# Optimization experiments

Measured on AMD Instinct MI355X. Metric: run time of the kernel, lower is better.

## Reference

```python
import jax, jax.numpy as jnp
import numpy as np

B, S, I, H = 1024, 1024, 32, 128

def setup_inputs() -> dict:
    key = jax.random.key(0)
    ks = jax.random.split(key, 10)
    def xavier(k, shape):
        fan_in, fan_out = shape
        bound = float(np.sqrt(6.0 / (fan_in + fan_out)))
        return jax.random.uniform(k, shape, jnp.float32, -bound, bound)
    return {
        "x": jax.random.normal(ks[0], (B, S, I), jnp.float32),
        "W_r": xavier(ks[1], (I, H)), "U_r": xavier(ks[2], (H, H)), "b_r": jnp.zeros((H,), jnp.float32),
        "W_z": xavier(ks[3], (I, H)), "U_z": xavier(ks[4], (H, H)), "b_z": jnp.zeros((H,), jnp.float32),
        "W_h": xavier(ks[5], (I, H)), "U_h": xavier(ks[6], (H, H)), "b_h": jnp.zeros((H,), jnp.float32),
    }

def reference(x, W_r, U_r, b_r, W_z, U_z, b_z, W_h, U_h, b_h):
    # x: [B, S, I]. Precompute all input projections in one big GEMM each (math-identical,
    # since x_t @ W is independent across t), then scan the sequential recurrence.
    xz = jnp.einsum('bsi,ih->bsh', x, W_z) + b_z  # [B,S,H]
    xh = jnp.einsum('bsi,ih->bsh', x, W_h) + b_h  # [B,S,H]
    # r_t = sigmoid(x@W_r + h@U_r + b_r) is computed in the original but never used
    # (h_tilde is NOT gated by r), so it has no effect on the output.

    h0 = jnp.zeros((x.shape[0], U_z.shape[0]), x.dtype)  # [B,H]

    def step(h, inp):
        xz_t, xh_t = inp  # each [B,H]
        z = jax.nn.sigmoid(xz_t + h @ U_z)
        hh = jnp.tanh(xh_t + h @ U_h)
        h_new = (1.0 - z) * h + z * hh  # note: swapped vs standard GRU, faithful to source
        return h_new, h_new

    # scan over time: [S,B,H]
    xs = (jnp.swapaxes(xz, 0, 1), jnp.swapaxes(xh, 0, 1))
    h_last, hs = jax.lax.scan(step, h0, xs)
    hidden_seq = jnp.swapaxes(hs, 0, 1)  # [B,S,H]
    return hidden_seq, h_last[None]  # final state keeps leading dim of 1, as in source
```

## Files before the change

### kernel.cpp

```cpp
#include <hip/hip_runtime.h>
#include <hip/hip_bf16.h>

typedef __bf16 bf16x8 __attribute__((ext_vector_type(8)));
typedef float  f32x4  __attribute__((ext_vector_type(4)));
typedef unsigned short u16;
typedef unsigned short u16x4 __attribute__((ext_vector_type(4)));
typedef unsigned long long u64;

#define NB 1024
#define NS 1024
#define NI 32
#define NH 128

__device__ __forceinline__ u64 pack4_bf16(f32x4 v) {
  u16x4 p;
#pragma unroll
  for (int r = 0; r < 4; ++r) p[r] = __builtin_bit_cast(u16, (__bf16)v[r]);
  return __builtin_bit_cast(u64, p);
}

__device__ __forceinline__ void lds_barrier() {
  __builtin_amdgcn_sched_barrier(0);
  asm volatile("s_waitcnt lgkmcnt(0)" ::: "memory");
  __builtin_amdgcn_s_barrier();
  asm volatile("" ::: "memory");
  __builtin_amdgcn_sched_barrier(0);
}

__global__ __launch_bounds__(512, 2) void gru_scan(
    const float* __restrict__ x,
    const float* __restrict__ Wz, const float* __restrict__ Uz, const float* __restrict__ bz,
    const float* __restrict__ Wh, const float* __restrict__ Uh, const float* __restrict__ bh,
    float* __restrict__ out)
{
  __shared__ __align__(16) u64 hb[2][16][17][2];
  __shared__ __align__(16) u64 hx[2][8][4][17][2];

  const int tid  = threadIdx.x;
  const int lane = tid & 63;
  const int w    = tid >> 6;
  const int ml   = lane & 15;
  const int g    = lane >> 4;
  const int rb   = blockIdx.x * 16;

  bf16x8 ufrag[2][4];
  bf16x8 wfrag[2];
  f32x4  bias2[2];
  {
    const float* Ug[2] = {Uz, Uh};
    const float* Wg[2] = {Wz, Wh};
    const float* bg[2] = {bz, bh};
    const int n0 = 16 * w + ml;
#pragma unroll
    for (int gate = 0; gate < 2; ++gate) {
#pragma unroll
      for (int kt = 0; kt < 4; ++kt)
#pragma unroll
        for (int j = 0; j < 8; ++j)
          ufrag[gate][kt][j] = (__bf16)Ug[gate][(32 * kt + 8 * g + j) * NH + n0];
#pragma unroll
      for (int j = 0; j < 8; ++j)
        wfrag[gate][j] = (__bf16)Wg[gate][(8 * g + j) * NH + n0];
      const int nb = 16 * w + 4 * g;
#pragma unroll
      for (int r = 0; r < 4; ++r) bias2[gate][r] = bg[gate][nb + r];
    }
  }

  for (int i = tid; i < 16 * 17 * 2; i += 512) ((u64*)hb[0])[i] = 0ULL;

  const int r_st  = tid >> 5;
  const int c8    = tid & 31;
  const int tt_st = c8 >> 2;
  const int ku_st = c8 & 3;
  const float* xbase = x + (size_t)(rb + r_st) * (NS * NI) + c8 * 8;

  {
    f32x4 a0 = *(const f32x4*)(xbase);
    f32x4 a1 = *(const f32x4*)(xbase + 4);
    bf16x8 u;
#pragma unroll
    for (int j = 0; j < 4; ++j) { u[j] = (__bf16)a0[j]; u[4 + j] = (__bf16)a1[j]; }
    *(bf16x8*)&hx[0][tt_st][ku_st][r_st][0] = u;
  }
  __syncthreads();

  const int woff_ku = 2 * w + (g >> 1);
  const int whalf   = g & 1;

  f32x4 hv = {0.f, 0.f, 0.f, 0.f};
  float* optr = out + (size_t)(rb + ml) * NS * NH + 16 * w + 4 * g;

  f32x4 vxa, vxb;
  const float NL2E  = -1.4426950408889634f;
  const float P2L2E =  2.8853900817779268f;
  const f32x4 zero4 = {0.f, 0.f, 0.f, 0.f};

  f32x4 axz, axh;
  {
    bf16x8 xf = *(const bf16x8*)&hx[0][0][g][ml][0];
    axz = __builtin_amdgcn_mfma_f32_16x16x32_bf16(wfrag[0], xf, bias2[0], 0, 0, 0);
    axh = __builtin_amdgcn_mfma_f32_16x16x32_bf16(wfrag[1], xf, bias2[1], 0, 0, 0);
  }

#define GRU_STEP(P, XB, TT)                                                                \
  {                                                                                        \
                      \
    bf16x8 hf0 = *(const bf16x8*)&hb[P][ 0 + g][ml][0];                                    \
    bf16x8 hf1 = *(const bf16x8*)&hb[P][ 4 + g][ml][0];                                    \
    bf16x8 hf2 = *(const bf16x8*)&hb[P][ 8 + g][ml][0];                                    \
    bf16x8 hf3 = *(const bf16x8*)&hb[P][12 + g][ml][0];                                    \
    const int nxb = ((TT) == 7) ? (XB) ^ 1 : (XB);                                         \
    const int ntt = ((TT) + 1) & 7;                                                        \
    bf16x8 xf = *(const bf16x8*)&hx[nxb][ntt][g][ml][0];                                   \
                                         \
    f32x4 z1 = __builtin_amdgcn_mfma_f32_16x16x32_bf16(ufrag[0][0], hf0, axz,   0, 0, 0);  \
    f32x4 h1 = __builtin_amdgcn_mfma_f32_16x16x32_bf16(ufrag[1][0], hf0, axh,   0, 0, 0);  \
    f32x4 z2 = __builtin_amdgcn_mfma_f32_16x16x32_bf16(ufrag[0][2], hf2, zero4, 0, 0, 0);  \
    f32x4 h2 = __builtin_amdgcn_mfma_f32_16x16x32_bf16(ufrag[1][2], hf2, zero4, 0, 0, 0);  \
    z1 = __builtin_amdgcn_mfma_f32_16x16x32_bf16(ufrag[0][1], hf1, z1, 0, 0, 0);           \
    h1 = __builtin_amdgcn_mfma_f32_16x16x32_bf16(ufrag[1][1], hf1, h1, 0, 0, 0);           \
    z2 = __builtin_amdgcn_mfma_f32_16x16x32_bf16(ufrag[0][3], hf3, z2, 0, 0, 0);           \
    h2 = __builtin_amdgcn_mfma_f32_16x16x32_bf16(ufrag[1][3], hf3, h2, 0, 0, 0);           \
                                    \
    axz = __builtin_amdgcn_mfma_f32_16x16x32_bf16(wfrag[0], xf, bias2[0], 0, 0, 0);        \
    axh = __builtin_amdgcn_mfma_f32_16x16x32_bf16(wfrag[1], xf, bias2[1], 0, 0, 0);        \
    const f32x4 az = z1 + z2;                                                              \
    const f32x4 ah = h1 + h2;                                                              \
                                        \
    f32x4 hn;                                                                              \
    _Pragma("unroll")                                                                      \
    for (int r = 0; r < 4; ++r) {                                                          \
      float ez = __builtin_amdgcn_exp2f(az[r] * NL2E);                                     \
      float zz = __builtin_amdgcn_rcpf(1.f + ez);                                          \
      float eh = __builtin_amdgcn_exp2f(ah[r] * P2L2E);                                    \
      float th = 1.f - 2.f * __builtin_amdgcn_rcpf(1.f + eh);                              \
      hn[r] = __builtin_fmaf(zz, th - hv[r], hv[r]);                                       \
    }                                                                                      \
    hv = hn;                                                                               \
                                              \
    hb[P ^ 1][woff_ku][ml][whalf] = pack4_bf16(hn);                                        \
                      \
    __builtin_nontemporal_store(hn, (f32x4*)optr);                                         \
    optr += NH;                                                                            \
  }

  for (int chunk = 0; chunk < NS / 8; ++chunk) {
    const int  xb   = chunk & 1;
    const bool more = (chunk + 1 < NS / 8);
#pragma unroll
    for (int tt = 0; tt < 8; ++tt) {
      if (tt == 0 && more) {
        const float* p = xbase + (size_t)(chunk + 1) * (8 * NI);
        vxa = *(const f32x4*)(p);
        vxb = *(const f32x4*)(p + 4);
      }

      if (tt & 1) { GRU_STEP(1, xb, tt) } else { GRU_STEP(0, xb, tt) }

      if (tt == 6 && more) {
        bf16x8 u;
#pragma unroll
        for (int j = 0; j < 4; ++j) { u[j] = (__bf16)vxa[j]; u[4 + j] = (__bf16)vxb[j]; }
        *(bf16x8*)&hx[xb ^ 1][tt_st][ku_st][r_st][0] = u;
      }

      lds_barrier();
    }
  }

  const size_t lbase = (size_t)NB * NS * NH + (size_t)(rb + ml) * NH + 16 * w + 4 * g;
  *(f32x4*)(out + lbase) = hv;
}

extern "C" void kernel_launch(void* const* d_in, const int* in_sizes, int n_in,
                              void* d_out, int out_size, void* d_ws, size_t ws_size,
                              hipStream_t stream) {
  const float* x  = (const float*)d_in[0];
  const float* Wz = (const float*)d_in[4];
  const float* Uz = (const float*)d_in[5];
  const float* bz = (const float*)d_in[6];
  const float* Wh = (const float*)d_in[7];
  const float* Uh = (const float*)d_in[8];
  const float* bh = (const float*)d_in[9];
  float* out = (float*)d_out;

  gru_scan<<<dim3(NB / 16), dim3(512), 0, stream>>>(x, Wz, Uz, bz, Wh, Uh, bh, out);
}
```

Before: 490.6 us.

## Halve block to 4 waves with two column tiles each and fuse gate math

Each block now runs 256 threads (4 waves), and each wave computes two 16-column output tiles per gate instead of one. The aim is cheaper per-step barriers and more MFMA work per wave to hide latency on the sequential scan. The gate math is rewritten to use a single reciprocal by combining sigmoid and tanh into one fraction, with inputs clamped to ±15 to avoid overflow. In exchange, each wave holds more register fragments and there are fewer waves per CU to overlap stalls.

Measured after the change: 572.9 us. +16.8%, slower.

```diff
diff --git a/kernel.cpp b/kernel.cpp
--- a/kernel.cpp
+++ b/kernel.cpp
@@ -27,7 +27,26 @@
   __builtin_amdgcn_sched_barrier(0);
 }
 
-__global__ __launch_bounds__(512, 2) void gru_scan(
+__device__ __forceinline__ f32x4 gru_elem(f32x4 az, f32x4 ah, f32x4 h) {
+  const float NL2E  = -1.4426950408889634f;
+  const float P2L2E =  2.8853900817779268f;
+  f32x4 hn;
+#pragma unroll
+  for (int r = 0; r < 4; ++r) {
+    float a  = fminf(15.f, fmaxf(-15.f, az[r]));
+    float b  = fminf(15.f, fmaxf(-15.f, ah[r]));
+    float e  = __builtin_amdgcn_exp2f(a * NL2E);
+    float f  = __builtin_amdgcn_exp2f(b * P2L2E);
+    float fp = f + 1.f;
+    float num = __builtin_fmaf(-h[r], fp, f - 1.f);
+    float den = (1.f + e) * fp;
+    float rr  = __builtin_amdgcn_rcpf(den);
+    hn[r] = __builtin_fmaf(num, rr, h[r]);
+  }
+  return hn;
+}
+
+__global__ __launch_bounds__(256, 1) void gru_scan(
     const float* __restrict__ x,
     const float* __restrict__ Wz, const float* __restrict__ Uz, const float* __restrict__ bz,
     const float* __restrict__ Wh, const float* __restrict__ Uh, const float* __restrict__ bh,
@@ -43,106 +62,119 @@
   const int g    = lane >> 4;
   const int rb   = blockIdx.x * 16;
 
-  bf16x8 ufrag[2][4];
-  bf16x8 wfrag[2];
-  f32x4  bias2[2];
+  bf16x8 ufrag[2][2][4];
+  bf16x8 wfrag[2][2];
+  f32x4  bias2[2][2];
   {
     const float* Ug[2] = {Uz, Uh};
     const float* Wg[2] = {Wz, Wh};
     const float* bg[2] = {bz, bh};
-    const int n0 = 16 * w + ml;
 #pragma unroll
     for (int gate = 0; gate < 2; ++gate) {
 #pragma unroll
-      for (int kt = 0; kt < 4; ++kt)
+      for (int nt = 0; nt < 2; ++nt) {
+        const int n0 = 32 * w + 16 * nt + ml;
+#pragma unroll
+        for (int kt = 0; kt < 4; ++kt)
+#pragma unroll
+          for (int j = 0; j < 8; ++j)
+            ufrag[gate][nt][kt][j] = (__bf16)Ug[gate][(32 * kt + 8 * g + j) * NH + n0];
 #pragma unroll
         for (int j = 0; j < 8; ++j)
-          ufrag[gate][kt][j] = (__bf16)Ug[gate][(32 * kt + 8 * g + j) * NH + n0];
-#pragma unroll
-      for (int j = 0; j < 8; ++j)
-        wfrag[gate][j] = (__bf16)Wg[gate][(8 * g + j) * NH + n0];
-      const int nb = 16 * w + 4 * g;
-#pragma unroll
-      for (int r = 0; r < 4; ++r) bias2[gate][r] = bg[gate][nb + r];
+          wfrag[gate][nt][j] = (__bf16)Wg[gate][(8 * g + j) * NH + n0];
+        const int nb = 32 * w + 16 * nt + 4 * g;
+#pragma unroll
+        for (int r = 0; r < 4; ++r) bias2[gate][nt][r] = bg[gate][nb + r];
+      }
     }
   }
 
-  for (int i = tid; i < 16 * 17 * 2; i += 512) ((u64*)hb[0])[i] = 0ULL;
-
-  const int r_st  = tid >> 5;
-  const int c8    = tid & 31;
-  const int tt_st = c8 >> 2;
-  const int ku_st = c8 & 3;
-  const float* xbase = x + (size_t)(rb + r_st) * (NS * NI) + c8 * 8;
+  for (int i = tid; i < 16 * 17 * 2; i += 256) ((u64*)hb[0])[i] = 0ULL;
+
+  const int r_st  = tid >> 4;
+  const int c16   = tid & 15;
+  const int tt_st = c16 >> 1;
+  const int ku0   = (c16 & 1) * 2;
+  const float* xbase = x + (size_t)(rb + r_st) * (NS * NI) + tt_st * NI + (c16 & 1) * 16;
 
   {
     f32x4 a0 = *(const f32x4*)(xbase);
     f32x4 a1 = *(const f32x4*)(xbase + 4);
-    bf16x8 u;
-#pragma unroll
-    for (int j = 0; j < 4; ++j) { u[j] = (__bf16)a0[j]; u[4 + j] = (__bf16)a1[j]; }
-    *(bf16x8*)&hx[0][tt_st][ku_st][r_st][0] = u;
+    f32x4 a2 = *(const f32x4*)(xbase + 8);
+    f32x4 a3 = *(const f32x4*)(xbase + 12);
+    bf16x8 u0, u1;
+#pragma unroll
+    for (int j = 0; j < 4; ++j) {
+      u0[j] = (__bf16)a0[j]; u0[4 + j] = (__bf16)a1[j];
+      u1[j] = (__bf16)a2[j]; u1[4 + j] = (__bf16)a3[j];
+    }
+    *(bf16x8*)&hx[0][tt_st][ku0 + 0][r_st][0] = u0;
+    *(bf16x8*)&hx[0][tt_st][ku0 + 1][r_st][0] = u1;
   }
   __syncthreads();
 
-  const int woff_ku = 2 * w + (g >> 1);
-  const int whalf   = g & 1;
-
-  f32x4 hv = {0.f, 0.f, 0.f, 0.f};
-  float* optr = out + (size_t)(rb + ml) * NS * NH + 16 * w + 4 * g;
-
-  f32x4 vxa, vxb;
-  const float NL2E  = -1.4426950408889634f;
-  const float P2L2E =  2.8853900817779268f;
+  f32x4 hv0 = {0.f, 0.f, 0.f, 0.f};
+  f32x4 hv1 = {0.f, 0.f, 0.f, 0.f};
+  float* optr = out + (size_t)(rb + ml) * NS * NH + 32 * w + 4 * g;
+
+  f32x4 vx0, vx1, vx2, vx3;
   const f32x4 zero4 = {0.f, 0.f, 0.f, 0.f};
 
-  f32x4 axz, axh;
+  f32x4 axz0, axz1, axh0, axh1;
   {
     bf16x8 xf = *(const bf16x8*)&hx[0][0][g][ml][0];
-    axz = __builtin_amdgcn_mfma_f32_16x16x32_bf16(wfrag[0], xf, bias2[0], 0, 0, 0);
-    axh = __builtin_amdgcn_mfma_f32_16x16x32_bf16(wfrag[1], xf, bias2[1], 0, 0, 0);
-  }
-
-#define GRU_STEP(P, XB, TT)                                                                \
-  {                                                                                        \
-                      \
-    bf16x8 hf0 = *(const bf16x8*)&hb[P][ 0 + g][ml][0];                                    \
-    bf16x8 hf1 = *(const bf16x8*)&hb[P][ 4 + g][ml][0];                                    \
-    bf16x8 hf2 = *(const bf16x8*)&hb[P][ 8 + g][ml][0];                                    \
-    bf16x8 hf3 = *(const bf16x8*)&hb[P][12 + g][ml][0];                                    \
-    const int nxb = ((TT) == 7) ? (XB) ^ 1 : (XB);                                         \
-    const int ntt = ((TT) + 1) & 7;                                                        \
-    bf16x8 xf = *(const bf16x8*)&hx[nxb][ntt][g][ml][0];                                   \
-                                         \
-    f32x4 z1 = __builtin_amdgcn_mfma_f32_16x16x32_bf16(ufrag[0][0], hf0, axz,   0, 0, 0);  \
-    f32x4 h1 = __builtin_amdgcn_mfma_f32_16x16x32_bf16(ufrag[1][0], hf0, axh,   0, 0, 0);  \
-    f32x4 z2 = __builtin_amdgcn_mfma_f32_16x16x32_bf16(ufrag[0][2], hf2, zero4, 0, 0, 0);  \
-    f32x4 h2 = __builtin_amdgcn_mfma_f32_16x16x32_bf16(ufrag[1][2], hf2, zero4, 0, 0, 0);  \
-    z1 = __builtin_amdgcn_mfma_f32_16x16x32_bf16(ufrag[0][1], hf1, z1, 0, 0, 0);           \
-    h1 = __builtin_amdgcn_mfma_f32_16x16x32_bf16(ufrag[1][1], hf1, h1, 0, 0, 0);           \
-    z2 = __builtin_amdgcn_mfma_f32_16x16x32_bf16(ufrag[0][3], hf3, z2, 0, 0, 0);           \
-    h2 = __builtin_amdgcn_mfma_f32_16x16x32_bf16(ufrag[1][3], hf3, h2, 0, 0, 0);           \
-                                    \
-    axz = __builtin_amdgcn_mfma_f32_16x16x32_bf16(wfrag[0], xf, bias2[0], 0, 0, 0);        \
-    axh = __builtin_amdgcn_mfma_f32_16x16x32_bf16(wfrag[1], xf, bias2[1], 0, 0, 0);        \
-    const f32x4 az = z1 + z2;                                                              \
-    const f32x4 ah = h1 + h2;                                                              \
-                                        \
-    f32x4 hn;                                                                              \
-    _Pragma("unroll")                                                                      \
-    for (int r = 0; r < 4; ++r) {                                                          \
-      float ez = __builtin_amdgcn_exp2f(az[r] * NL2E);                                     \
-      float zz = __builtin_amdgcn_rcpf(1.f + ez);                                          \
-      float eh = __builtin_amdgcn_exp2f(ah[r] * P2L2E);                                    \
-      float th = 1.f - 2.f * __builtin_amdgcn_rcpf(1.f + eh);                              \
-      hn[r] = __builtin_fmaf(zz, th - hv[r], hv[r]);                                       \
-    }                                                                                      \
-    hv = hn;                                                                               \
-                                              \
-    hb[P ^ 1][woff_ku][ml][whalf] = pack4_bf16(hn);                                        \
-                      \
-    __builtin_nontemporal_store(hn, (f32x4*)optr);                                         \
-    optr += NH;                                                                            \
+    axz0 = __builtin_amdgcn_mfma_f32_16x16x32_bf16(wfrag[0][0], xf, bias2[0][0], 0, 0, 0);
+    axz1 = __builtin_amdgcn_mfma_f32_16x16x32_bf16(wfrag[0][1], xf, bias2[0][1], 0, 0, 0);
+    axh0 = __builtin_amdgcn_mfma_f32_16x16x32_bf16(wfrag[1][0], xf, bias2[1][0], 0, 0, 0);
+    axh1 = __builtin_amdgcn_mfma_f32_16x16x32_bf16(wfrag[1][1], xf, bias2[1][1], 0, 0, 0);
+  }
+
+#define GRU_STEP(P, XB, TT)                                                                 \
+  {                                                                                         \
+                       \
+    bf16x8 hf0 = *(const bf16x8*)&hb[P][ 0 + g][ml][0];                                     \
+    bf16x8 hf1 = *(const bf16x8*)&hb[P][ 4 + g][ml][0];                                     \
+    bf16x8 hf2 = *(const bf16x8*)&hb[P][ 8 + g][ml][0];                                     \
+    bf16x8 hf3 = *(const bf16x8*)&hb[P][12 + g][ml][0];                                     \
+    const int nxb = ((TT) == 7) ? (XB) ^ 1 : (XB);                                          \
+    const int ntt = ((TT) + 1) & 7;                                                         \
+    bf16x8 xf = *(const bf16x8*)&hx[nxb][ntt][g][ml][0];                                    \
+                 \
+    f32x4 cz0a = __builtin_amdgcn_mfma_f32_16x16x32_bf16(ufrag[0][0][0], hf0, axz0, 0,0,0); \
+    f32x4 cz1a = __builtin_amdgcn_mfma_f32_16x16x32_bf16(ufrag[0][1][0], hf0, axz1, 0,0,0); \
+    f32x4 ch0a = __builtin_amdgcn_mfma_f32_16x16x32_bf16(ufrag[1][0][0], hf0, axh0, 0,0,0); \
+    f32x4 ch1a = __builtin_amdgcn_mfma_f32_16x16x32_bf16(ufrag[1][1][0], hf0, axh1, 0,0,0); \
+    f32x4 cz0b = __builtin_amdgcn_mfma_f32_16x16x32_bf16(ufrag[0][0][2], hf2, zero4, 0,0,0);\
+    f32x4 cz1b = __builtin_amdgcn_mfma_f32_16x16x32_bf16(ufrag[0][1][2], hf2, zero4, 0,0,0);\
+    f32x4 ch0b = __builtin_amdgcn_mfma_f32_16x16x32_bf16(ufrag[1][0][2], hf2, zero4, 0,0,0);\
+    f32x4 ch1b = __builtin_amdgcn_mfma_f32_16x16x32_bf16(ufrag[1][1][2], hf2, zero4, 0,0,0);\
+    cz0a = __builtin_amdgcn_mfma_f32_16x16x32_bf16(ufrag[0][0][1], hf1, cz0a, 0, 0, 0);     \
+    cz1a = __builtin_amdgcn_mfma_f32_16x16x32_bf16(ufrag[0][1][1], hf1, cz1a, 0, 0, 0);     \
+    ch0a = __builtin_amdgcn_mfma_f32_16x16x32_bf16(ufrag[1][0][1], hf1, ch0a, 0, 0, 0);     \
+    ch1a = __builtin_amdgcn_mfma_f32_16x16x32_bf16(ufrag[1][1][1], hf1, ch1a, 0, 0, 0);     \
+    cz0b = __builtin_amdgcn_mfma_f32_16x16x32_bf16(ufrag[0][0][3], hf3, cz0b, 0, 0, 0);     \
+    cz1b = __builtin_amdgcn_mfma_f32_16x16x32_bf16(ufrag[0][1][3], hf3, cz1b, 0, 0, 0);     \
+    ch0b = __builtin_amdgcn_mfma_f32_16x16x32_bf16(ufrag[1][0][3], hf3, ch0b, 0, 0, 0);     \
+    ch1b = __builtin_amdgcn_mfma_f32_16x16x32_bf16(ufrag[1][1][3], hf3, ch1b, 0, 0, 0);     \
+                                           \
+    axz0 = __builtin_amdgcn_mfma_f32_16x16x32_bf16(wfrag[0][0], xf, bias2[0][0], 0, 0, 0);  \
+    axz1 = __builtin_amdgcn_mfma_f32_16x16x32_bf16(wfrag[0][1], xf, bias2[0][1], 0, 0, 0);  \
+    axh0 = __builtin_amdgcn_mfma_f32_16x16x32_bf16(wfrag[1][0], xf, bias2[1][0], 0, 0, 0);  \
+    axh1 = __builtin_amdgcn_mfma_f32_16x16x32_bf16(wfrag[1][1], xf, bias2[1][1], 0, 0, 0);  \
+    const f32x4 az0 = cz0a + cz0b;                                                          \
+    const f32x4 az1 = cz1a + cz1b;                                                          \
+    const f32x4 ah0 = ch0a + ch0b;                                                          \
+    const f32x4 ah1 = ch1a + ch1b;                                                          \
+    f32x4 hn0 = gru_elem(az0, ah0, hv0);                                                    \
+    f32x4 hn1 = gru_elem(az1, ah1, hv1);                                                    \
+    hv0 = hn0; hv1 = hn1;                                                                   \
+                          \
+    hb[P ^ 1][4 * w + 0 + (g >> 1)][ml][g & 1] = pack4_bf16(hn0);                           \
+    hb[P ^ 1][4 * w + 2 + (g >> 1)][ml][g & 1] = pack4_bf16(hn1);                           \
+                       \
+    __builtin_nontemporal_store(hn0, (f32x4*)optr);                                         \
+    __builtin_nontemporal_store(hn1, (f32x4*)(optr + 16));                                  \
+    optr += NH;                                                                             \
   }
 
   for (int chunk = 0; chunk < NS / 8; ++chunk) {
@@ -152,25 +184,32 @@
     for (int tt = 0; tt < 8; ++tt) {
       if (tt == 0 && more) {
         const float* p = xbase + (size_t)(chunk + 1) * (8 * NI);
-        vxa = *(const f32x4*)(p);
-        vxb = *(const f32x4*)(p + 4);
+        vx0 = *(const f32x4*)(p);
+        vx1 = *(const f32x4*)(p + 4);
+        vx2 = *(const f32x4*)(p + 8);
+        vx3 = *(const f32x4*)(p + 12);
       }
 
       if (tt & 1) { GRU_STEP(1, xb, tt) } else { GRU_STEP(0, xb, tt) }
 
       if (tt == 6 && more) {
-        bf16x8 u;
-#pragma unroll
-        for (int j = 0; j < 4; ++j) { u[j] = (__bf16)vxa[j]; u[4 + j] = (__bf16)vxb[j]; }
-        *(bf16x8*)&hx[xb ^ 1][tt_st][ku_st][r_st][0] = u;
+        bf16x8 u0, u1;
+#pragma unroll
+        for (int j = 0; j < 4; ++j) {
+          u0[j] = (__bf16)vx0[j]; u0[4 + j] = (__bf16)vx1[j];
+          u1[j] = (__bf16)vx2[j]; u1[4 + j] = (__bf16)vx3[j];
+        }
+        *(bf16x8*)&hx[xb ^ 1][tt_st][ku0 + 0][r_st][0] = u0;
+        *(bf16x8*)&hx[xb ^ 1][tt_st][ku0 + 1][r_st][0] = u1;
       }
 
       lds_barrier();
     }
   }
 
-  const size_t lbase = (size_t)NB * NS * NH + (size_t)(rb + ml) * NH + 16 * w + 4 * g;
-  *(f32x4*)(out + lbase) = hv;
+  const size_t lbase = (size_t)NB * NS * NH + (size_t)(rb + ml) * NH + 32 * w + 4 * g;
+  *(f32x4*)(out + lbase)      = hv0;
+  *(f32x4*)(out + lbase + 16) = hv1;
 }
 
 extern "C" void kernel_launch(void* const* d_in, const int* in_sizes, int n_in,
@@ -185,5 +224,5 @@
   const float* bh = (const float*)d_in[9];
   float* out = (float*)d_out;
 
-  gru_scan<<<dim3(NB / 16), dim3(512), 0, stream>>>(x, Wz, Uz, bz, Wh, Uh, bh, out);
-}
+  gru_scan<<<dim3(NB / 16), dim3(256), 0, stream>>>(x, Wz, Uz, bz, Wh, Uh, bh, out);
+}
```

## Load x directly into per-lane registers and drop LDS staging buffer

Applied to the files above, without the earlier changes.

Removes the shared-memory staging of x chunks. Each lane now loads its own x fragment from global memory into register arrays, double-buffered across chunks, and converts to bf16 interleaved with the recurrence steps. The gate math is rewritten to clamp pre-activations and combine the two reciprocals into one, and launch bounds are relaxed to one block per CU so the larger register footprint fits. Each lane now issues redundant global x loads across the eight waves, and the clamped gate math changes numerics slightly.

Measured after the change: 668.1 us. +36.2%, slower.

```diff
diff --git a/kernel.cpp b/kernel.cpp
--- a/kernel.cpp
+++ b/kernel.cpp
@@ -11,12 +11,20 @@
 #define NS 1024
 #define NI 32
 #define NH 128
+#define NCH (NS / 8)
 
 __device__ __forceinline__ u64 pack4_bf16(f32x4 v) {
   u16x4 p;
 #pragma unroll
   for (int r = 0; r < 4; ++r) p[r] = __builtin_bit_cast(u16, (__bf16)v[r]);
   return __builtin_bit_cast(u64, p);
+}
+
+__device__ __forceinline__ bf16x8 cvt8(f32x4 a, f32x4 b) {
+  bf16x8 u;
+#pragma unroll
+  for (int j = 0; j < 4; ++j) { u[j] = (__bf16)a[j]; u[4 + j] = (__bf16)b[j]; }
+  return u;
 }
 
 __device__ __forceinline__ void lds_barrier() {
@@ -27,14 +35,32 @@
   __builtin_amdgcn_sched_barrier(0);
 }
 
-__global__ __launch_bounds__(512, 2) void gru_scan(
+__device__ __forceinline__ f32x4 gru_elem(f32x4 az, f32x4 ah, f32x4 h) {
+  const float NL2E  = -1.4426950408889634f;
+  const float P2L2E =  2.8853900817779268f;
+  f32x4 hn;
+#pragma unroll
+  for (int r = 0; r < 4; ++r) {
+    float a  = fminf(15.f, fmaxf(-15.f, az[r]));
+    float b  = fminf(15.f, fmaxf(-15.f, ah[r]));
+    float e  = __builtin_amdgcn_exp2f(a * NL2E);
+    float f  = __builtin_amdgcn_exp2f(b * P2L2E);
+    float fp = f + 1.f;
+    float num = __builtin_fmaf(-h[r], fp, f - 1.f);
+    float den = (1.f + e) * fp;
+    float rr  = __builtin_amdgcn_rcpf(den);
+    hn[r] = __builtin_fmaf(num, rr, h[r]);
+  }
+  return hn;
+}
+
+__global__ __launch_bounds__(512, 1) void gru_scan(
     const float* __restrict__ x,
     const float* __restrict__ Wz, const float* __restrict__ Uz, const float* __restrict__ bz,
     const float* __restrict__ Wh, const float* __restrict__ Uh, const float* __restrict__ bh,
     float* __restrict__ out)
 {
   __shared__ __align__(16) u64 hb[2][16][17][2];
-  __shared__ __align__(16) u64 hx[2][8][4][17][2];
 
   const int tid  = threadIdx.x;
   const int lane = tid & 63;
@@ -69,51 +95,36 @@
 
   for (int i = tid; i < 16 * 17 * 2; i += 512) ((u64*)hb[0])[i] = 0ULL;
 
-  const int r_st  = tid >> 5;
-  const int c8    = tid & 31;
-  const int tt_st = c8 >> 2;
-  const int ku_st = c8 & 3;
-  const float* xbase = x + (size_t)(rb + r_st) * (NS * NI) + c8 * 8;
-
-  {
-    f32x4 a0 = *(const f32x4*)(xbase);
-    f32x4 a1 = *(const f32x4*)(xbase + 4);
-    bf16x8 u;
-#pragma unroll
-    for (int j = 0; j < 4; ++j) { u[j] = (__bf16)a0[j]; u[4 + j] = (__bf16)a1[j]; }
-    *(bf16x8*)&hx[0][tt_st][ku_st][r_st][0] = u;
-  }
-  __syncthreads();
-
-  const int woff_ku = 2 * w + (g >> 1);
-  const int whalf   = g & 1;
+  const float* xrow = x + (size_t)(rb + ml) * (NS * NI) + 8 * g;
 
   f32x4 hv = {0.f, 0.f, 0.f, 0.f};
   float* optr = out + (size_t)(rb + ml) * NS * NH + 16 * w + 4 * g;
-
-  f32x4 vxa, vxb;
-  const float NL2E  = -1.4426950408889634f;
-  const float P2L2E =  2.8853900817779268f;
   const f32x4 zero4 = {0.f, 0.f, 0.f, 0.f};
 
+  bf16x8 XA[8], XB[8];
   f32x4 axz, axh;
+
   {
-    bf16x8 xf = *(const bf16x8*)&hx[0][0][g][ml][0];
-    axz = __builtin_amdgcn_mfma_f32_16x16x32_bf16(wfrag[0], xf, bias2[0], 0, 0, 0);
-    axh = __builtin_amdgcn_mfma_f32_16x16x32_bf16(wfrag[1], xf, bias2[1], 0, 0, 0);
-  }
-
-#define GRU_STEP(P, XB, TT)                                                                \
+    f32x4 ra[16];
+#pragma unroll
+    for (int q = 0; q < 8; ++q) {
+      const f32x4* p = (const f32x4*)(xrow + (size_t)q * NI);
+      ra[2 * q] = p[0]; ra[2 * q + 1] = p[1];
+    }
+#pragma unroll
+    for (int q = 0; q < 8; ++q) XA[q] = cvt8(ra[2 * q], ra[2 * q + 1]);
+    axz = __builtin_amdgcn_mfma_f32_16x16x32_bf16(wfrag[0], XA[0], bias2[0], 0, 0, 0);
+    axh = __builtin_amdgcn_mfma_f32_16x16x32_bf16(wfrag[1], XA[0], bias2[1], 0, 0, 0);
+  }
+
+  __syncthreads();
+
+#define GRU_STEP(P, XF)                                                                    \
   {                                                                                        \
-                      \
     bf16x8 hf0 = *(const bf16x8*)&hb[P][ 0 + g][ml][0];                                    \
     bf16x8 hf1 = *(const bf16x8*)&hb[P][ 4 + g][ml][0];                                    \
     bf16x8 hf2 = *(const bf16x8*)&hb[P][ 8 + g][ml][0];                                    \
     bf16x8 hf3 = *(const bf16x8*)&hb[P][12 + g][ml][0];                                    \
-    const int nxb = ((TT) == 7) ? (XB) ^ 1 : (XB);                                         \
-    const int ntt = ((TT) + 1) & 7;                                                        \
-    bf16x8 xf = *(const bf16x8*)&hx[nxb][ntt][g][ml][0];                                   \
-                                         \
     f32x4 z1 = __builtin_amdgcn_mfma_f32_16x16x32_bf16(ufrag[0][0], hf0, axz,   0, 0, 0);  \
     f32x4 h1 = __builtin_amdgcn_mfma_f32_16x16x32_bf16(ufrag[1][0], hf0, axh,   0, 0, 0);  \
     f32x4 z2 = __builtin_amdgcn_mfma_f32_16x16x32_bf16(ufrag[0][2], hf2, zero4, 0, 0, 0);  \
@@ -122,51 +133,61 @@
     h1 = __builtin_amdgcn_mfma_f32_16x16x32_bf16(ufrag[1][1], hf1, h1, 0, 0, 0);           \
     z2 = __builtin_amdgcn_mfma_f32_16x16x32_bf16(ufrag[0][3], hf3, z2, 0, 0, 0);           \
     h2 = __builtin_amdgcn_mfma_f32_16x16x32_bf16(ufrag[1][3], hf3, h2, 0, 0, 0);           \
-                                    \
-    axz = __builtin_amdgcn_mfma_f32_16x16x32_bf16(wfrag[0], xf, bias2[0], 0, 0, 0);        \
-    axh = __builtin_amdgcn_mfma_f32_16x16x32_bf16(wfrag[1], xf, bias2[1], 0, 0, 0);        \
+    axz = __builtin_amdgcn_mfma_f32_16x16x32_bf16(wfrag[0], XF, bias2[0], 0, 0, 0);        \
+    axh = __builtin_amdgcn_mfma_f32_16x16x32_bf16(wfrag[1], XF, bias2[1], 0, 0, 0);        \
     const f32x4 az = z1 + z2;                                                              \
     const f32x4 ah = h1 + h2;                                                              \
-                                        \
-    f32x4 hn;                                                                              \
-    _Pragma("unroll")                                                                      \
-    for (int r = 0; r < 4; ++r) {                                                          \
-      float ez = __builtin_amdgcn_exp2f(az[r] * NL2E);                                     \
-      float zz = __builtin_amdgcn_rcpf(1.f + ez);                                          \
-      float eh = __builtin_amdgcn_exp2f(ah[r] * P2L2E);                                    \
-      float th = 1.f - 2.f * __builtin_amdgcn_rcpf(1.f + eh);                              \
-      hn[r] = __builtin_fmaf(zz, th - hv[r], hv[r]);                                       \
-    }                                                                                      \
+    f32x4 hn = gru_elem(az, ah, hv);                                                       \
     hv = hn;                                                                               \
-                                              \
-    hb[P ^ 1][woff_ku][ml][whalf] = pack4_bf16(hn);                                        \
-                      \
+    hb[P ^ 1][2 * w + (g >> 1)][ml][g & 1] = pack4_bf16(hn);                               \
     __builtin_nontemporal_store(hn, (f32x4*)optr);                                         \
     optr += NH;                                                                            \
   }
 
-  for (int chunk = 0; chunk < NS / 8; ++chunk) {
-    const int  xb   = chunk & 1;
-    const bool more = (chunk + 1 < NS / 8);
-#pragma unroll
-    for (int tt = 0; tt < 8; ++tt) {
-      if (tt == 0 && more) {
-        const float* p = xbase + (size_t)(chunk + 1) * (8 * NI);
-        vxa = *(const f32x4*)(p);
-        vxb = *(const f32x4*)(p + 4);
-      }
-
-      if (tt & 1) { GRU_STEP(1, xb, tt) } else { GRU_STEP(0, xb, tt) }
-
-      if (tt == 6 && more) {
-        bf16x8 u;
-#pragma unroll
-        for (int j = 0; j < 4; ++j) { u[j] = (__bf16)vxa[j]; u[4 + j] = (__bf16)vxb[j]; }
-        *(bf16x8*)&hx[xb ^ 1][tt_st][ku_st][r_st][0] = u;
-      }
-
-      lds_barrier();
-    }
+#define CHUNK_BODY(XC, XN, CIDX)                                                           \
+  {                                                                                        \
+    const int c1 = ((CIDX) + 1 < NCH) ? (CIDX) + 1 : (CIDX);                               \
+    const float* xp = xrow + (size_t)c1 * (8 * NI);                                        \
+    f32x4 rA[8], rB[8];                                                                    \
+    GRU_STEP(0, XC[1])                                                                     \
+    _Pragma("unroll")                                                                      \
+    for (int q = 0; q < 4; ++q) {                                                          \
+      const f32x4* p = (const f32x4*)(xp + (size_t)q * NI);                                \
+      rA[2 * q] = p[0]; rA[2 * q + 1] = p[1];                                              \
+    }                                                                                      \
+    lds_barrier();                                                                         \
+    GRU_STEP(1, XC[2])                                                                     \
+    lds_barrier();                                                                         \
+    GRU_STEP(0, XC[3])                                                                     \
+    XN[0] = cvt8(rA[0], rA[1]);                                                            \
+    lds_barrier();                                                                         \
+    GRU_STEP(1, XC[4])                                                                     \
+    XN[1] = cvt8(rA[2], rA[3]);                                                            \
+    lds_barrier();                                                                         \
+    GRU_STEP(0, XC[5])                                                                     \
+    _Pragma("unroll")                                                                      \
+    for (int q = 0; q < 4; ++q) {                                                          \
+      const f32x4* p = (const f32x4*)(xp + (size_t)(4 + q) * NI);                          \
+      rB[2 * q] = p[0]; rB[2 * q + 1] = p[1];                                              \
+    }                                                                                      \
+    XN[2] = cvt8(rA[4], rA[5]);                                                            \
+    lds_barrier();                                                                         \
+    GRU_STEP(1, XC[6])                                                                     \
+    XN[3] = cvt8(rA[6], rA[7]);                                                            \
+    lds_barrier();                                                                         \
+    GRU_STEP(0, XC[7])                                                                     \
+    XN[4] = cvt8(rB[0], rB[1]);                                                            \
+    XN[5] = cvt8(rB[2], rB[3]);                                                            \
+    lds_barrier();                                                                         \
+    GRU_STEP(1, XN[0])                                                                     \
+    XN[6] = cvt8(rB[4], rB[5]);                                                            \
+    XN[7] = cvt8(rB[6], rB[7]);                                                            \
+    lds_barrier();                                                                         \
+  }
+
+  for (int p = 0; p < NCH / 2; ++p) {
+    CHUNK_BODY(XA, XB, 2 * p)
+    CHUNK_BODY(XB, XA, 2 * p + 1)
   }
 
   const size_t lbase = (size_t)NB * NS * NH + (size_t)(rb + ml) * NH + 16 * w + 4 * g;
```

## Swizzle LDS layouts, defer output stores, and fuse gate math into one reciprocal

Applied to the files above, without the earlier changes.

Replaces the padded LDS buffers for hidden state and x with XOR-swizzled layouts to avoid bank conflicts without padding. Each step's global output store is deferred to the next step and issued before its MFMAs, so the store overlaps the matrix work, and x staging moves inside the step. The sigmoid/tanh update is rewritten with one combined reciprocal and clamped inputs, cutting transcendental ops on the serial critical path. The chunk loop is split by buffer parity so buffer indices are compile-time constants, at the cost of larger code and slightly different numerics from the clamp.

New measurement: 500.8 us. 1.02x slower.

```diff
diff --git a/kernel.cpp b/kernel.cpp
--- a/kernel.cpp
+++ b/kernel.cpp
@@ -27,14 +27,33 @@
   __builtin_amdgcn_sched_barrier(0);
 }
 
+__device__ __forceinline__ f32x4 gru_elem(f32x4 az, f32x4 ah, f32x4 h) {
+  const float NL2E  = -1.4426950408889634f;
+  const float P2L2E =  2.8853900817779268f;
+  f32x4 hn;
+#pragma unroll
+  for (int r = 0; r < 4; ++r) {
+    float a  = fminf(15.f, fmaxf(-15.f, az[r]));
+    float b  = fminf(15.f, fmaxf(-15.f, ah[r]));
+    float e  = __builtin_amdgcn_exp2f(a * NL2E);
+    float f  = __builtin_amdgcn_exp2f(b * P2L2E);
+    float fp = f + 1.f;
+    float num = __builtin_fmaf(-h[r], fp, f - 1.f);
+    float den = (1.f + e) * fp;
+    float rr  = __builtin_amdgcn_rcpf(den);
+    hn[r] = __builtin_fmaf(num, rr, h[r]);
+  }
+  return hn;
+}
+
 __global__ __launch_bounds__(512, 2) void gru_scan(
     const float* __restrict__ x,
     const float* __restrict__ Wz, const float* __restrict__ Uz, const float* __restrict__ bz,
     const float* __restrict__ Wh, const float* __restrict__ Uh, const float* __restrict__ bh,
     float* __restrict__ out)
 {
-  __shared__ __align__(16) u64 hb[2][16][17][2];
-  __shared__ __align__(16) u64 hx[2][8][4][17][2];
+  __shared__ __align__(16) u64    hbuf[2][16][32];
+  __shared__ __align__(16) bf16x8 xbuf[2][8][16][4];
 
   const int tid  = threadIdx.x;
   const int lane = tid & 63;
@@ -67,12 +86,12 @@
     }
   }
 
-  for (int i = tid; i < 16 * 17 * 2; i += 512) ((u64*)hb[0])[i] = 0ULL;
+  for (int i = tid; i < 16 * 32; i += 512) hbuf[0][i >> 5][i & 31] = 0ULL;
 
   const int r_st  = tid >> 5;
   const int c8    = tid & 31;
   const int tt_st = c8 >> 2;
-  const int ku_st = c8 & 3;
+  const int un_st = (c8 & 3) ^ (r_st & 3);
   const float* xbase = x + (size_t)(rb + r_st) * (NS * NI) + c8 * 8;
 
   {
@@ -81,94 +100,103 @@
     bf16x8 u;
 #pragma unroll
     for (int j = 0; j < 4; ++j) { u[j] = (__bf16)a0[j]; u[4 + j] = (__bf16)a1[j]; }
-    *(bf16x8*)&hx[0][tt_st][ku_st][r_st][0] = u;
+    xbuf[0][tt_st][r_st][un_st] = u;
   }
   __syncthreads();
 
-  const int woff_ku = 2 * w + (g >> 1);
-  const int whalf   = g & 1;
+  const int sw = (ml & 7) << 1;
+  int ridx[4];
+#pragma unroll
+  for (int kt = 0; kt < 4; ++kt) ridx[kt] = (8 * kt + 2 * g) ^ sw;
+  const int widx = (4 * w + g) ^ sw;
+  const int xidx = g ^ (ml & 3);
 
   f32x4 hv = {0.f, 0.f, 0.f, 0.f};
   float* optr = out + (size_t)(rb + ml) * NS * NH + 16 * w + 4 * g;
 
   f32x4 vxa, vxb;
-  const float NL2E  = -1.4426950408889634f;
-  const float P2L2E =  2.8853900817779268f;
   const f32x4 zero4 = {0.f, 0.f, 0.f, 0.f};
 
   f32x4 axz, axh;
   {
-    bf16x8 xf = *(const bf16x8*)&hx[0][0][g][ml][0];
+    bf16x8 xf = xbuf[0][0][ml][xidx];
     axz = __builtin_amdgcn_mfma_f32_16x16x32_bf16(wfrag[0], xf, bias2[0], 0, 0, 0);
     axh = __builtin_amdgcn_mfma_f32_16x16x32_bf16(wfrag[1], xf, bias2[1], 0, 0, 0);
   }
 
-#define GRU_STEP(P, XB, TT)                                                                \
+#define GRU_STEP(P, XB, TT, DO_STORE, DO_STAGE)                                            \
   {                                                                                        \
-                      \
-    bf16x8 hf0 = *(const bf16x8*)&hb[P][ 0 + g][ml][0];                                    \
-    bf16x8 hf1 = *(const bf16x8*)&hb[P][ 4 + g][ml][0];                                    \
-    bf16x8 hf2 = *(const bf16x8*)&hb[P][ 8 + g][ml][0];                                    \
-    bf16x8 hf3 = *(const bf16x8*)&hb[P][12 + g][ml][0];                                    \
-    const int nxb = ((TT) == 7) ? (XB) ^ 1 : (XB);                                         \
+                 \
+    const u64* hrow = &hbuf[P][ml][0];                                                     \
+    bf16x8 hf0 = *(const bf16x8*)(hrow + ridx[0]);                                         \
+    bf16x8 hf1 = *(const bf16x8*)(hrow + ridx[1]);                                         \
+    bf16x8 hf2 = *(const bf16x8*)(hrow + ridx[2]);                                         \
+    bf16x8 hf3 = *(const bf16x8*)(hrow + ridx[3]);                                         \
+    const int nb_ = ((TT) == 7) ? (XB) ^ 1 : (XB);                                         \
     const int ntt = ((TT) + 1) & 7;                                                        \
-    bf16x8 xf = *(const bf16x8*)&hx[nxb][ntt][g][ml][0];                                   \
-                                         \
+    bf16x8 xf = xbuf[nb_][ntt][ml][xidx];                                                  \
+                     \
+    if (DO_STORE) { __builtin_nontemporal_store(hv, (f32x4*)optr); optr += NH; }           \
+            \
+    if (DO_STAGE) {                                                                        \
+      bf16x8 u;                                                                            \
+      _Pragma("unroll")                                                                    \
+      for (int j = 0; j < 4; ++j) { u[j] = (__bf16)vxa[j]; u[4 + j] = (__bf16)vxb[j]; }    \
+      xbuf[(XB) ^ 1][tt_st][r_st][un_st] = u;                                              \
+    }                                                                                      \
+                                 \
     f32x4 z1 = __builtin_amdgcn_mfma_f32_16x16x32_bf16(ufrag[0][0], hf0, axz,   0, 0, 0);  \
+    f32x4 z2 = __builtin_amdgcn_mfma_f32_16x16x32_bf16(ufrag[0][2], hf2, zero4, 0, 0, 0);  \
+    z1 = __builtin_amdgcn_mfma_f32_16x16x32_bf16(ufrag[0][1], hf1, z1, 0, 0, 0);           \
+    z2 = __builtin_amdgcn_mfma_f32_16x16x32_bf16(ufrag[0][3], hf3, z2, 0, 0, 0);           \
     f32x4 h1 = __builtin_amdgcn_mfma_f32_16x16x32_bf16(ufrag[1][0], hf0, axh,   0, 0, 0);  \
-    f32x4 z2 = __builtin_amdgcn_mfma_f32_16x16x32_bf16(ufrag[0][2], hf2, zero4, 0, 0, 0);  \
     f32x4 h2 = __builtin_amdgcn_mfma_f32_16x16x32_bf16(ufrag[1][2], hf2, zero4, 0, 0, 0);  \
-    z1 = __builtin_amdgcn_mfma_f32_16x16x32_bf16(ufrag[0][1], hf1, z1, 0, 0, 0);           \
     h1 = __builtin_amdgcn_mfma_f32_16x16x32_bf16(ufrag[1][1], hf1, h1, 0, 0, 0);           \
-    z2 = __builtin_amdgcn_mfma_f32_16x16x32_bf16(ufrag[0][3], hf3, z2, 0, 0, 0);           \
     h2 = __builtin_amdgcn_mfma_f32_16x16x32_bf16(ufrag[1][3], hf3, h2, 0, 0, 0);           \
-                                    \
+                             \
     axz = __builtin_amdgcn_mfma_f32_16x16x32_bf16(wfrag[0], xf, bias2[0], 0, 0, 0);        \
     axh = __builtin_amdgcn_mfma_f32_16x16x32_bf16(wfrag[1], xf, bias2[1], 0, 0, 0);        \
+                                                                 \
     const f32x4 az = z1 + z2;                                                              \
     const f32x4 ah = h1 + h2;                                                              \
-                                        \
-    f32x4 hn;                                                                              \
-    _Pragma("unroll")                                                                      \
-    for (int r = 0; r < 4; ++r) {                                                          \
-      float ez = __builtin_amdgcn_exp2f(az[r] * NL2E);                                     \
-      float zz = __builtin_amdgcn_rcpf(1.f + ez);                                          \
-      float eh = __builtin_amdgcn_exp2f(ah[r] * P2L2E);                                    \
-      float th = 1.f - 2.f * __builtin_amdgcn_rcpf(1.f + eh);                              \
-      hn[r] = __builtin_fmaf(zz, th - hv[r], hv[r]);                                       \
-    }                                                                                      \
+    f32x4 hn = gru_elem(az, ah, hv);                                                       \
     hv = hn;                                                                               \
-                                              \
-    hb[P ^ 1][woff_ku][ml][whalf] = pack4_bf16(hn);                                        \
-                      \
-    __builtin_nontemporal_store(hn, (f32x4*)optr);                                         \
-    optr += NH;                                                                            \
+                                       \
+    hbuf[P ^ 1][ml][widx] = pack4_bf16(hn);                                                \
+    lds_barrier();                                                                         \
   }
 
   for (int chunk = 0; chunk < NS / 8; ++chunk) {
     const int  xb   = chunk & 1;
     const bool more = (chunk + 1 < NS / 8);
-#pragma unroll
-    for (int tt = 0; tt < 8; ++tt) {
-      if (tt == 0 && more) {
-        const float* p = xbase + (size_t)(chunk + 1) * (8 * NI);
-        vxa = *(const f32x4*)(p);
-        vxb = *(const f32x4*)(p + 4);
-      }
-
-      if (tt & 1) { GRU_STEP(1, xb, tt) } else { GRU_STEP(0, xb, tt) }
-
-      if (tt == 6 && more) {
-        bf16x8 u;
-#pragma unroll
-        for (int j = 0; j < 4; ++j) { u[j] = (__bf16)vxa[j]; u[4 + j] = (__bf16)vxb[j]; }
-        *(bf16x8*)&hx[xb ^ 1][tt_st][ku_st][r_st][0] = u;
-      }
-
-      lds_barrier();
+    const bool st0  = (chunk > 0);
+
+    if (xb == 0) {
+      if (more) { const float* p = xbase + (size_t)(chunk + 1) * (8 * NI);
+                  vxa = *(const f32x4*)(p); vxb = *(const f32x4*)(p + 4); }
+      GRU_STEP(0, 0, 0, st0,  false)
+      GRU_STEP(1, 0, 1, true, false)
+      GRU_STEP(0, 0, 2, true, false)
+      GRU_STEP(1, 0, 3, true, false)
+      GRU_STEP(0, 0, 4, true, false)
+      GRU_STEP(1, 0, 5, true, false)
+      GRU_STEP(0, 0, 6, true, more)
+      GRU_STEP(1, 0, 7, true, false)
+    } else {
+      if (more) { const float* p = xbase + (size_t)(chunk + 1) * (8 * NI);
+                  vxa = *(const f32x4*)(p); vxb = *(const f32x4*)(p + 4); }
+      GRU_STEP(0, 1, 0, true, false)
+      GRU_STEP(1, 1, 1, true, false)
+      GRU_STEP(0, 1, 2, true, false)
+      GRU_STEP(1, 1, 3, true, false)
+      GRU_STEP(0, 1, 4, true, false)
+      GRU_STEP(1, 1, 5, true, false)
+      GRU_STEP(0, 1, 6, true, more)
+      GRU_STEP(1, 1, 7, true, false)
     }
   }
 
+  __builtin_nontemporal_store(hv, (f32x4*)optr);
   const size_t lbase = (size_t)NB * NS * NH + (size_t)(rb + ml) * NH + 16 * w + 4 * g;
   *(f32x4*)(out + lbase) = hv;
 }
```
